# Performance work log

Measured on AMD Instinct MI355X. Metric: run time of the kernel, lower is better.

Reference implementation:

```python
import jax, jax.numpy as jnp
import numpy as np

N, E, G, L, D = 50000, 800000, 512, 3, 128
BN_EPS = 1e-5


def setup_inputs() -> dict:
    key = jax.random.key(0)
    ks = jax.random.split(key, 16)
    x = jax.random.normal(ks[0], (N, D), dtype=jnp.float32)
    edge_index = jax.random.randint(ks[1], (2, E), 0, N)
    batch = jnp.sort(jax.random.randint(ks[2], (N,), 0, G))
    W1 = jax.random.normal(ks[3], (L, D, D), dtype=jnp.float32) * 0.05
    b1 = jax.random.normal(ks[4], (L, D), dtype=jnp.float32) * 0.05
    gamma = jax.random.uniform(ks[5], (L, D), dtype=jnp.float32) + 0.5
    beta = jax.random.normal(ks[6], (L, D), dtype=jnp.float32) * 0.05
    running_mean = jax.random.normal(ks[7], (L, D), dtype=jnp.float32) * 0.1
    running_var = jax.random.uniform(ks[8], (L, D), dtype=jnp.float32) + 0.5
    W2 = jax.random.normal(ks[9], (L, D, D), dtype=jnp.float32) * 0.05
    b2 = jax.random.normal(ks[10], (L, D), dtype=jnp.float32) * 0.05
    lin1_W = jax.random.normal(ks[11], (L * D, L * D), dtype=jnp.float32) * 0.05
    lin1_b = jax.random.normal(ks[12], (L * D,), dtype=jnp.float32) * 0.05
    lin2_W = jax.random.normal(ks[13], (L * D, 10), dtype=jnp.float32) * 0.05
    lin2_b = jax.random.normal(ks[14], (10,), dtype=jnp.float32) * 0.05
    return {"x": x, "edge_index": edge_index, "batch": batch,
            "W1": W1, "b1": b1, "gamma": gamma, "beta": beta,
            "running_mean": running_mean, "running_var": running_var,
            "W2": W2, "b2": b2, "lin1_W": lin1_W, "lin1_b": lin1_b,
            "lin2_W": lin2_W, "lin2_b": lin2_b}


def _gin_layer(h, src, dst, W1, b1, gamma, beta, rm, rv, W2, b2):
    # GINConv (eps=0): MLP((1+eps)*x + sum_{j->i} x_j); aggregate src->dst
    agg = jax.ops.segment_sum(h[src], dst, num_segments=N)  # [N, D]
    z = (h + agg) @ W1 + b1
    # BatchNorm1d in eval mode (running stats)
    z = (z - rm) * (gamma / jnp.sqrt(rv + BN_EPS)) + beta
    z = jax.nn.relu(z)
    return jax.nn.relu(z @ W2 + b2)


def reference(x, edge_index, batch, W1, b1, gamma, beta, running_mean,
              running_var, W2, b2, lin1_W, lin1_b, lin2_W, lin2_b):
    src, dst = edge_index[0], edge_index[1]
    h = x
    pooled = []
    for i in range(L):
        h = _gin_layer(h, src, dst, W1[i], b1[i], gamma[i], beta[i],
                       running_mean[i], running_var[i], W2[i], b2[i])
        pooled.append(jax.ops.segment_sum(h, batch, num_segments=G))  # [G, D]
    g = jnp.concatenate(pooled, axis=1)  # [G, L*D]
    g = jax.nn.relu(g @ lin1_W + lin1_b)
    # dropout is identity in eval mode
    return g @ lin2_W + lin2_b  # [G, num_classes]
```

## Files before the change

kernel.cpp:

```cpp
#include <hip/hip_runtime.h>
#include <hip/hip_bf16.h>

#define D_FEAT 128
#define N_GRAPHS 512
#define N_LAYERS 3
#define POOL_DIM (N_LAYERS * D_FEAT)
#define N_CLASSES 10
#define BN_EPS 1e-5f
#define CAP 64
#define NBINS 8
#define SLABCAP 768
#define NSLICE 4


typedef __attribute__((ext_vector_type(8))) short bf16x8;
typedef __attribute__((ext_vector_type(8))) unsigned short ushort8;
typedef __attribute__((ext_vector_type(4))) float f32x4;

__device__ __forceinline__ unsigned short f2bf(float f) {
    unsigned u = __builtin_bit_cast(unsigned, f);
    u += 0x7FFFu + ((u >> 16) & 1u);
    return (unsigned short)(u >> 16);
}
__device__ __forceinline__ float bf2f(unsigned short h) {
    unsigned u = ((unsigned)h) << 16;
    return __builtin_bit_cast(float, u);
}
__device__ __forceinline__ float bf_lo(unsigned u) {
    return __builtin_bit_cast(float, u << 16);
}
__device__ __forceinline__ float bf_hi(unsigned u) {
    return __builtin_bit_cast(float, u & 0xffff0000u);
}

__global__ __launch_bounds__(256) void setup_kernel(
        const float* __restrict__ x, unsigned short* __restrict__ xb,
        const float* __restrict__ W1, const float* __restrict__ W2,
        unsigned short* __restrict__ Wt,
        const float* __restrict__ b1, const float* __restrict__ gamma,
        const float* __restrict__ beta, const float* __restrict__ rm,
        const float* __restrict__ rv, const float* __restrict__ b2,
        float* __restrict__ ea, float* __restrict__ eb,
        int* __restrict__ cursor, float* __restrict__ pooled,
        const int* __restrict__ ei, int2* __restrict__ pairs,
        int* __restrict__ cnts, int E,
        int N, int n4, int B0, int B1, int B2, int B3, int B4) {
    int b = blockIdx.x, tid = threadIdx.x;
    if (b < B0) {
        int i = b * 256 + tid;
        if (i < n4) {
            float4 v = ((const float4*)x)[i];
            ushort4 o;
            o.x = f2bf(v.x); o.y = f2bf(v.y); o.z = f2bf(v.z); o.w = f2bf(v.w);
            int node = i >> 5;
            int c4 = i & 31;
            int sl = c4 >> 3;
            int off = c4 & 7;
            ((ushort4*)xb)[((size_t)sl * N + node) * 8 + off] = o;
        }
    } else if (b < B1) {
        __shared__ float tile[64][65];
        int t = b - B0;
        int slot = t >> 2;
        int r0 = ((t >> 1) & 1) * 64;
        int c0 = (t & 1) * 64;
        int l = slot >> 1;
        const float* W = (slot & 1) ? W2 : W1;
        const float* Wb = W + (size_t)l * D_FEAT * D_FEAT;
        int rr = tid >> 2, cc4 = (tid & 3) * 16;
        #pragma unroll
        for (int j = 0; j < 16; ++j)
            tile[rr][cc4 + j] = Wb[(size_t)(r0 + rr) * D_FEAT + c0 + cc4 + j];
        __syncthreads();
        int nn = tid >> 2, kk4 = (tid & 3) * 16;
        unsigned short* Wo = Wt + (size_t)slot * D_FEAT * D_FEAT;
        #pragma unroll
        for (int j = 0; j < 16; ++j)
            Wo[(size_t)(c0 + nn) * D_FEAT + r0 + kk4 + j] = f2bf(tile[kk4 + j][nn]);
    } else if (b < B2) {
        int i = (b - B1) * 256 + tid;
        if (i < N_LAYERS * D_FEAT) {
            int l = i >> 7, c = i & 127;
            float s = gamma[i] * rsqrtf(rv[i] + BN_EPS);
            ea[(2 * l) * D_FEAT + c] = s;
            eb[(2 * l) * D_FEAT + c] = (b1[i] - rm[i]) * s + beta[i];
            ea[(2 * l + 1) * D_FEAT + c] = 1.0f;
            eb[(2 * l + 1) * D_FEAT + c] = b2[i];
        }
    } else if (b < B3) {
        int i = (b - B2) * 256 + tid;
        if (i < N) cursor[i] = 0;
    } else if (b < B4) {
        int i = (b - B3) * 256 + tid;
        if (i < N_GRAPHS * POOL_DIM) pooled[i] = 0.f;
    } else {
        __shared__ int loc[NBINS];
        int bb = b - B4;
        int per = (E + 255) / 256;
        int e0 = bb * per;
        int e1 = e0 + per; if (e1 > E) e1 = E;
        int span = (N + NBINS - 1) / NBINS;
        if (tid < NBINS) loc[tid] = 0;
        __syncthreads();
        for (int e = e0 + tid; e < e1; e += 256) {
            int dst = ei[E + e];
            int src = ei[e];
            int bin = dst / span;
            int p = atomicAdd(&loc[bin], 1);
            if (p < SLABCAP)
                pairs[((size_t)(bin * 256 + bb)) * SLABCAP + p] = make_int2(src, dst);
        }
        __syncthreads();
        if (tid < NBINS)
            cnts[tid * 256 + bb] = loc[tid];
    }
}

__global__ __launch_bounds__(256) void fill_v3(const int2* __restrict__ pairs,
                                               const int* __restrict__ cnts,
                                               int* __restrict__ cursor,
                                               unsigned short* __restrict__ bucket) {
    int r = blockIdx.x & 7;
    int chunk = blockIdx.x >> 3;
    #pragma unroll
    for (int s = 0; s < 4; ++s) {
        int blk = chunk * 4 + s;
        int cnt = cnts[r * 256 + blk];
        if (cnt > SLABCAP) cnt = SLABCAP;
        const int2* slab = pairs + (size_t)(r * 256 + blk) * SLABCAP;
        for (int p = threadIdx.x; p < cnt; p += 256) {
            int2 pr = slab[p];
            int pos = atomicAdd(&cursor[pr.y], 1);
            if (pos < CAP)
                bucket[(size_t)pr.y * CAP + pos] = (unsigned short)pr.x;
        }
    }
}

__global__ __launch_bounds__(256) void agg_slice(
        const unsigned short* __restrict__ hs,
        const int* __restrict__ deg,
        const unsigned short* __restrict__ bucket,
        unsigned short* __restrict__ ys,
        int n, int nchunks) {
    int xcd = blockIdx.x & 7;
    int s = xcd >> 1;
    int chunk = (blockIdx.x >> 3) * 2 + (xcd & 1);
    if (chunk >= nchunks) return;
    int wave = threadIdx.x >> 6, lane = threadIdx.x & 63;
    int grp = lane >> 2, sub = lane & 3;
    int n0 = chunk * 64 + wave * 16 + grp;
    bool valid = n0 < n;
    int node = valid ? n0 : 0;
    int d = valid ? deg[node] : 0;
    if (d > CAP) d = CAP;

    const uint4* h4 = (const uint4*)hs;
    size_t sbase = (size_t)s * n * 4;
    const unsigned short* brow = bucket + (size_t)node * CAP;

    int dmax = d;
    dmax = max(dmax, __shfl_xor(dmax, 4));
    dmax = max(dmax, __shfl_xor(dmax, 8));
    dmax = max(dmax, __shfl_xor(dmax, 16));
    dmax = max(dmax, __shfl_xor(dmax, 32));

    uint4 sv = h4[sbase + (size_t)node * 4 + sub];

    float acc[8] = {0.f,0.f,0.f,0.f,0.f,0.f,0.f,0.f};

    if (dmax > 0) {
        int sA[4];
        #pragma unroll
        for (int u = 0; u < 4; ++u) {
            sA[u] = node;
            if (u < d) sA[u] = (int)brow[u];
        }
        for (int t = 0; t < dmax; t += 4) {
            uint4 w[4];
            #pragma unroll
            for (int u = 0; u < 4; ++u) {
                w[u] = make_uint4(0u, 0u, 0u, 0u);
                if (t + u < d)
                    w[u] = h4[sbase + (size_t)sA[u] * 4 + sub];
            }
            int sB[4];
            #pragma unroll
            for (int u = 0; u < 4; ++u) {
                int e = t + 4 + u;
                sB[u] = node;
                if (e < d) sB[u] = (int)brow[e];
            }
            #pragma unroll
            for (int u = 0; u < 4; ++u) {
                uint4 v = w[u];
                acc[0] += bf_lo(v.x); acc[1] += bf_hi(v.x);
                acc[2] += bf_lo(v.y); acc[3] += bf_hi(v.y);
                acc[4] += bf_lo(v.z); acc[5] += bf_hi(v.z);
                acc[6] += bf_lo(v.w); acc[7] += bf_hi(v.w);
            }
            #pragma unroll
            for (int u = 0; u < 4; ++u) sA[u] = sB[u];
        }
    }

    acc[0] += bf_lo(sv.x); acc[1] += bf_hi(sv.x);
    acc[2] += bf_lo(sv.y); acc[3] += bf_hi(sv.y);
    acc[4] += bf_lo(sv.z); acc[5] += bf_hi(sv.z);
    acc[6] += bf_lo(sv.w); acc[7] += bf_hi(sv.w);

    if (valid) {
        uint4 o;
        o.x = (unsigned)f2bf(acc[0]) | ((unsigned)f2bf(acc[1]) << 16);
        o.y = (unsigned)f2bf(acc[2]) | ((unsigned)f2bf(acc[3]) << 16);
        o.z = (unsigned)f2bf(acc[4]) | ((unsigned)f2bf(acc[5]) << 16);
        o.w = (unsigned)f2bf(acc[6]) | ((unsigned)f2bf(acc[7]) << 16);
        ((uint4*)ys)[sbase + (size_t)node * 4 + sub] = o;
    }
}

__global__ __launch_bounds__(256) void layer_fused(const unsigned short* __restrict__ A,
                                                   const unsigned short* __restrict__ Wt1,
                                                   const unsigned short* __restrict__ Wt2,
                                                   const float* __restrict__ ea1,
                                                   const float* __restrict__ eb1,
                                                   const float* __restrict__ ea2,
                                                   const float* __restrict__ eb2,
                                                   const int* __restrict__ batch,
                                                   float* __restrict__ pooled, int loff,
                                                   unsigned short* __restrict__ outh, int n) {
    __shared__ unsigned short As[64][136];
    __shared__ unsigned short Ws[128][136];
    int tid = threadIdx.x;
    int row0 = blockIdx.x * 64;
    int wave = tid >> 6, lane = tid & 63;
    int m0 = wave * 16;
    int lrow = lane & 15, lq = lane >> 4;

    #pragma unroll
    for (int i = 0; i < 4; ++i) {
        int idx = tid + i * 256;
        int r = idx >> 4, c = (idx & 15) * 8;
        int sl = c >> 5, off = c & 31;
        ushort8 v = (ushort8)0;
        if (row0 + r < n)
            v = *(const ushort8*)&A[((size_t)sl * n + (row0 + r)) * 32 + off];
        *(ushort8*)&As[r][c] = v;
    }
    #pragma unroll
    for (int i = 0; i < 8; ++i) {
        int idx = tid + i * 256;
        int r = idx >> 4, c = (idx & 15) * 8;
        *(ushort8*)&Ws[r][c] = *(const ushort8*)&Wt1[(size_t)r * D_FEAT + c];
    }

    ushort8 w2reg[8];
    #pragma unroll
    for (int i = 0; i < 8; ++i) {
        int idx = tid + i * 256;
        int r = idx >> 4, c = (idx & 15) * 8;
        w2reg[i] = *(const ushort8*)&Wt2[(size_t)r * D_FEAT + c];
    }

    int gr0 = row0 + m0 + lq * 4;
    int bq[4];
    if (gr0 + 3 < n) {
        int4 b4 = *(const int4*)&batch[gr0];
        bq[0] = b4.x; bq[1] = b4.y; bq[2] = b4.z; bq[3] = b4.w;
    } else {
        #pragma unroll
        for (int r = 0; r < 4; ++r)
            bq[r] = (gr0 + r < n) ? batch[gr0 + r] : -1;
    }
    __syncthreads();

    f32x4 acc[8] = {};
    #pragma unroll
    for (int t = 0; t < 4; ++t) {
        bf16x8 a = *(const bf16x8*)&As[m0 + lrow][t * 32 + lq * 8];
        #pragma unroll
        for (int nt = 0; nt < 8; ++nt) {
            bf16x8 b = *(const bf16x8*)&Ws[nt * 16 + lrow][t * 32 + lq * 8];
            acc[nt] = __builtin_amdgcn_mfma_f32_16x16x32_bf16(a, b, acc[nt], 0, 0, 0);
        }
    }
    __syncthreads();

    #pragma unroll
    for (int nt = 0; nt < 8; ++nt) {
        int col = nt * 16 + lrow;
        float al = ea1[col], be = eb1[col];
        #pragma unroll
        for (int r = 0; r < 4; ++r) {
            float v = fmaxf(fmaf(acc[nt][r], al, be), 0.f);
            As[m0 + lq * 4 + r][col] = f2bf(v);
        }
    }
    #pragma unroll
    for (int i = 0; i < 8; ++i) {
        int idx = tid + i * 256;
        int r = idx >> 4, c = (idx & 15) * 8;
        *(ushort8*)&Ws[r][c] = w2reg[i];
    }
    __syncthreads();

    f32x4 acc2[8] = {};
    #pragma unroll
    for (int t = 0; t < 4; ++t) {
        bf16x8 a = *(const bf16x8*)&As[m0 + lrow][t * 32 + lq * 8];
        #pragma unroll
        for (int nt = 0; nt < 8; ++nt) {
            bf16x8 b = *(const bf16x8*)&Ws[nt * 16 + lrow][t * 32 + lq * 8];
            acc2[nt] = __builtin_amdgcn_mfma_f32_16x16x32_bf16(a, b, acc2[nt], 0, 0, 0);
        }
    }

    float vv[8][4];
    #pragma unroll
    for (int nt = 0; nt < 8; ++nt) {
        int col = nt * 16 + lrow;
        float al = ea2[col], be = eb2[col];
        int sl = col >> 5, off = col & 31;
        #pragma unroll
        for (int r = 0; r < 4; ++r) {
            unsigned short hb = f2bf(fmaxf(fmaf(acc2[nt][r], al, be), 0.f));
            vv[nt][r] = bf2f(hb);
            if (outh) {
                int grow = row0 + m0 + lq * 4 + r;
                if (grow < n)
                    outh[((size_t)sl * n + grow) * 32 + off] = hb;
            }
        }
    }

    int gmn = 0x7fffffff, gmx = -1;
    #pragma unroll
    for (int r = 0; r < 4; ++r) {
        if (bq[r] >= 0) {
            gmn = bq[r] < gmn ? bq[r] : gmn;
            gmx = bq[r] > gmx ? bq[r] : gmx;
        }
    }
    {
        int t;
        t = __shfl_xor(gmn, 16); gmn = t < gmn ? t : gmn;
        t = __shfl_xor(gmn, 32); gmn = t < gmn ? t : gmn;
        t = __shfl_xor(gmx, 16); gmx = t > gmx ? t : gmx;
        t = __shfl_xor(gmx, 32); gmx = t > gmx ? t : gmx;
    }
    for (int seg = gmn; seg <= gmx; ++seg) {
        #pragma unroll
        for (int nt = 0; nt < 8; ++nt) {
            float s = 0.f;
            #pragma unroll
            for (int r = 0; r < 4; ++r)
                if (bq[r] == seg) s += vv[nt][r];
            s += __shfl_xor(s, 16);
            s += __shfl_xor(s, 32);
            if (lq == 0 && s != 0.f)
                atomicAdd(&pooled[(size_t)seg * POOL_DIM + loff + nt * 16 + lrow], s);
        }
    }
}

__global__ __launch_bounds__(384) void head_kernel(const float* __restrict__ pooled,
                                                   const float* __restrict__ W1,
                                                   const float* __restrict__ b1v,
                                                   const float* __restrict__ W2,
                                                   const float* __restrict__ b2v,
                                                   float* __restrict__ out) {
    __shared__ float f1[4][POOL_DIM];
    int j = threadIdx.x;
    int g0 = blockIdx.x * 4;
    const float* pr = pooled + (size_t)g0 * POOL_DIM;
    float bb = b1v[j];
    float s0 = bb, s1 = bb, s2 = bb, s3 = bb;
    for (int k0 = 0; k0 < POOL_DIM; k0 += 8) {
        float w[8];
        #pragma unroll
        for (int i = 0; i < 8; ++i)
            w[i] = W1[(size_t)(k0 + i) * POOL_DIM + j];
        #pragma unroll
        for (int i = 0; i < 8; ++i) {
            int k = k0 + i;
            s0 = fmaf(pr[k],                w[i], s0);
            s1 = fmaf(pr[POOL_DIM + k],     w[i], s1);
            s2 = fmaf(pr[2 * POOL_DIM + k], w[i], s2);
            s3 = fmaf(pr[3 * POOL_DIM + k], w[i], s3);
        }
    }
    f1[0][j] = fmaxf(s0, 0.f);
    f1[1][j] = fmaxf(s1, 0.f);
    f1[2][j] = fmaxf(s2, 0.f);
    f1[3][j] = fmaxf(s3, 0.f);
    __syncthreads();
    if (j < 4 * N_CLASSES) {
        int g = j / N_CLASSES, c = j % N_CLASSES;
        float s = b2v[c];
        for (int k = 0; k < POOL_DIM; ++k)
            s = fmaf(f1[g][k], W2[(size_t)k * N_CLASSES + c], s);
        out[(size_t)(g0 + g) * N_CLASSES + c] = s;
    }
}

extern "C" void kernel_launch(void* const* d_in, const int* in_sizes, int n_in,
                              void* d_out, int out_size, void* d_ws, size_t ws_size,
                              hipStream_t stream) {
    const float* x      = (const float*)d_in[0];
    const int*   ei     = (const int*)  d_in[1];
    const int*   batch  = (const int*)  d_in[2];
    const float* W1     = (const float*)d_in[3];
    const float* b1     = (const float*)d_in[4];
    const float* gamma  = (const float*)d_in[5];
    const float* beta   = (const float*)d_in[6];
    const float* rm     = (const float*)d_in[7];
    const float* rv     = (const float*)d_in[8];
    const float* W2     = (const float*)d_in[9];
    const float* b2     = (const float*)d_in[10];
    const float* lin1W  = (const float*)d_in[11];
    const float* lin1b  = (const float*)d_in[12];
    const float* lin2W  = (const float*)d_in[13];
    const float* lin2b  = (const float*)d_in[14];
    float* out = (float*)d_out;

    const int N = in_sizes[0] / D_FEAT;
    const int E = in_sizes[1] / 2;

    char* ws = (char*)d_ws;
    auto carve = [&](size_t bytes) {
        char* p = ws;
        ws += (bytes + 255) & ~(size_t)255;
        return p;
    };
    int*   cursor    = (int*)  carve((size_t)N * 4);
    int*   cnts      = (int*)  carve((size_t)NBINS * 256 * 4);
    unsigned short* bucket = (unsigned short*)carve((size_t)N * CAP * 2);
    int2*  pairs     = (int2*) carve((size_t)NBINS * 256 * SLABCAP * 8);
    float* ea        = (float*)carve((size_t)2 * N_LAYERS * D_FEAT * 4);
    float* eb        = (float*)carve((size_t)2 * N_LAYERS * D_FEAT * 4);
    unsigned short* Wt   = (unsigned short*)carve((size_t)2 * N_LAYERS * D_FEAT * D_FEAT * 2);
    unsigned short* xb   = (unsigned short*)carve((size_t)N * D_FEAT * 2);
    unsigned short* ybuf = (unsigned short*)carve((size_t)N * D_FEAT * 2);
    unsigned short* hbuf = (unsigned short*)carve((size_t)N * D_FEAT * 2);
    float* pooled    = (float*)carve((size_t)N_GRAPHS * POOL_DIM * 4);

    const int n4 = N * D_FEAT / 4;
    const int B0 = (n4 + 255) / 256;
    const int B1 = B0 + 24;
    const int B2 = B1 + 2;
    const int B3 = B2 + (N + 255) / 256;
    const int B4 = B3 + (N_GRAPHS * POOL_DIM + 255) / 256;
    const int B5 = B4 + 256;

    setup_kernel<<<B5, 256, 0, stream>>>(x, xb, W1, W2, Wt, b1, gamma, beta,
                                         rm, rv, b2, ea, eb, cursor, pooled,
                                         ei, pairs, cnts, E,
                                         N, n4, B0, B1, B2, B3, B4);
    fill_v3<<<8 * 64, 256, 0, stream>>>(pairs, cnts, cursor, bucket);

    const int nchunks = (N + 63) / 64;
    const int gblocks = 8 * ((nchunks + 1) / 2);

    const unsigned short* hprev = xb;
    for (int l = 0; l < N_LAYERS; ++l) {
        agg_slice<<<gblocks, 256, 0, stream>>>(hprev, cursor, bucket, ybuf,
                                               N, nchunks);
        unsigned short* outh = (l == N_LAYERS - 1) ? nullptr : hbuf;
        layer_fused<<<(N + 63) / 64, 256, 0, stream>>>(ybuf,
                      Wt + (size_t)(2 * l) * D_FEAT * D_FEAT,
                      Wt + (size_t)(2 * l + 1) * D_FEAT * D_FEAT,
                      ea + (size_t)(2 * l) * D_FEAT,
                      eb + (size_t)(2 * l) * D_FEAT,
                      ea + (size_t)(2 * l + 1) * D_FEAT,
                      eb + (size_t)(2 * l + 1) * D_FEAT,
                      batch, pooled, l * D_FEAT, outh, N);
        hprev = hbuf;
    }
    head_kernel<<<N_GRAPHS / 4, 384, 0, stream>>>(pooled, lin1W, lin1b, lin2W, lin2b, out);
}
```

Measured before the change: 349.6 us.

## Use persistent grid in aggregation and load neighbor indices with one vector load plus shuffles

The aggregation kernel now runs a fixed grid of 2048 blocks that loop over chunks in a grid-stride fashion, keeping the XCD-to-slice mapping. Each lane loads 8 bucket indices with a single 16-byte load, and the first 32 neighbor ids are spread across the 4-lane group with shuffles, replacing scalar per-edge index loads. Degrees above 32 fall back to a serial scalar loop. The goal is to cut index-load latency and block launch overhead, at the cost of a serial tail and slightly more register pressure.

```diff
diff --git a/kernel.cpp b/kernel.cpp
--- a/kernel.cpp
+++ b/kernel.cpp
@@ -145,51 +145,44 @@
         int n, int nchunks) {
     int xcd = blockIdx.x & 7;
     int s = xcd >> 1;
-    int chunk = (blockIdx.x >> 3) * 2 + (xcd & 1);
-    if (chunk >= nchunks) return;
+    int worker = (blockIdx.x >> 3) * 2 + (xcd & 1);
     int wave = threadIdx.x >> 6, lane = threadIdx.x & 63;
     int grp = lane >> 2, sub = lane & 3;
-    int n0 = chunk * 64 + wave * 16 + grp;
-    bool valid = n0 < n;
-    int node = valid ? n0 : 0;
-    int d = valid ? deg[node] : 0;
-    if (d > CAP) d = CAP;
-
     const uint4* h4 = (const uint4*)hs;
     size_t sbase = (size_t)s * n * 4;
-    const unsigned short* brow = bucket + (size_t)node * CAP;
-
-    int dmax = d;
-    dmax = max(dmax, __shfl_xor(dmax, 4));
-    dmax = max(dmax, __shfl_xor(dmax, 8));
-    dmax = max(dmax, __shfl_xor(dmax, 16));
-    dmax = max(dmax, __shfl_xor(dmax, 32));
-
-    uint4 sv = h4[sbase + (size_t)node * 4 + sub];
-
-    float acc[8] = {0.f,0.f,0.f,0.f,0.f,0.f,0.f,0.f};
-
-    if (dmax > 0) {
-        int sA[4];
-        #pragma unroll
-        for (int u = 0; u < 4; ++u) {
-            sA[u] = node;
-            if (u < d) sA[u] = (int)brow[u];
-        }
-        for (int t = 0; t < dmax; t += 4) {
+
+    for (int chunk = worker; chunk < nchunks; chunk += 512) {
+        int n0 = chunk * 64 + wave * 16 + grp;
+        bool valid = n0 < n;
+        int node = valid ? n0 : 0;
+        int d = valid ? deg[node] : 0;
+        if (d > CAP) d = CAP;
+        const unsigned short* brow = bucket + (size_t)node * CAP;
+
+        uint4 iv = *(const uint4*)&brow[sub * 8];
+
+        uint4 sv = h4[sbase + (size_t)node * 4 + sub];
+
+        int dmax = d;
+        dmax = max(dmax, __shfl_xor(dmax, 4));
+        dmax = max(dmax, __shfl_xor(dmax, 8));
+        dmax = max(dmax, __shfl_xor(dmax, 16));
+        dmax = max(dmax, __shfl_xor(dmax, 32));
+
+        float acc[8] = {0.f,0.f,0.f,0.f,0.f,0.f,0.f,0.f};
+
+        auto do4 = [&](int e0, unsigned q0, unsigned q1) {
+            int id[4];
+            id[0] = (int)(q0 & 0xffffu);
+            id[1] = (int)(q0 >> 16);
+            id[2] = (int)(q1 & 0xffffu);
+            id[3] = (int)(q1 >> 16);
             uint4 w[4];
             #pragma unroll
             for (int u = 0; u < 4; ++u) {
                 w[u] = make_uint4(0u, 0u, 0u, 0u);
-                if (t + u < d)
-                    w[u] = h4[sbase + (size_t)sA[u] * 4 + sub];
-            }
-            int sB[4];
-            #pragma unroll
-            for (int u = 0; u < 4; ++u) {
-                int e = t + 4 + u;
-                sB[u] = node;
-                if (e < d) sB[u] = (int)brow[e];
+                if (e0 + u < d)
+                    w[u] = h4[sbase + (size_t)id[u] * 4 + sub];
             }
             #pragma unroll
             for (int u = 0; u < 4; ++u) {
@@ -199,23 +192,40 @@
                 acc[4] += bf_lo(v.z); acc[5] += bf_hi(v.z);
                 acc[6] += bf_lo(v.w); acc[7] += bf_hi(v.w);
             }
-            #pragma unroll
-            for (int u = 0; u < 4; ++u) sA[u] = sB[u];
-        }
-    }
-
-    acc[0] += bf_lo(sv.x); acc[1] += bf_hi(sv.x);
-    acc[2] += bf_lo(sv.y); acc[3] += bf_hi(sv.y);
-    acc[4] += bf_lo(sv.z); acc[5] += bf_hi(sv.z);
-    acc[6] += bf_lo(sv.w); acc[7] += bf_hi(sv.w);
-
-    if (valid) {
-        uint4 o;
-        o.x = (unsigned)f2bf(acc[0]) | ((unsigned)f2bf(acc[1]) << 16);
-        o.y = (unsigned)f2bf(acc[2]) | ((unsigned)f2bf(acc[3]) << 16);
-        o.z = (unsigned)f2bf(acc[4]) | ((unsigned)f2bf(acc[5]) << 16);
-        o.w = (unsigned)f2bf(acc[6]) | ((unsigned)f2bf(acc[7]) << 16);
-        ((uint4*)ys)[sbase + (size_t)node * 4 + sub] = o;
+        };
+
+        int dcap = dmax < 32 ? dmax : 32;
+        for (int t = 0; t < dcap; t += 8) {
+            int src = (grp << 2) + (t >> 3);
+            unsigned q0 = (unsigned)__shfl((int)iv.x, src);
+            unsigned q1 = (unsigned)__shfl((int)iv.y, src);
+            do4(t, q0, q1);
+            q0 = (unsigned)__shfl((int)iv.z, src);
+            q1 = (unsigned)__shfl((int)iv.w, src);
+            do4(t + 4, q0, q1);
+        }
+        for (int e = 32; e < d; ++e) {
+            int idx = (int)brow[e];
+            uint4 v = h4[sbase + (size_t)idx * 4 + sub];
+            acc[0] += bf_lo(v.x); acc[1] += bf_hi(v.x);
+            acc[2] += bf_lo(v.y); acc[3] += bf_hi(v.y);
+            acc[4] += bf_lo(v.z); acc[5] += bf_hi(v.z);
+            acc[6] += bf_lo(v.w); acc[7] += bf_hi(v.w);
+        }
+
+        acc[0] += bf_lo(sv.x); acc[1] += bf_hi(sv.x);
+        acc[2] += bf_lo(sv.y); acc[3] += bf_hi(sv.y);
+        acc[4] += bf_lo(sv.z); acc[5] += bf_hi(sv.z);
+        acc[6] += bf_lo(sv.w); acc[7] += bf_hi(sv.w);
+
+        if (valid) {
+            uint4 o;
+            o.x = (unsigned)f2bf(acc[0]) | ((unsigned)f2bf(acc[1]) << 16);
+            o.y = (unsigned)f2bf(acc[2]) | ((unsigned)f2bf(acc[3]) << 16);
+            o.z = (unsigned)f2bf(acc[4]) | ((unsigned)f2bf(acc[5]) << 16);
+            o.w = (unsigned)f2bf(acc[6]) | ((unsigned)f2bf(acc[7]) << 16);
+            ((uint4*)ys)[sbase + (size_t)node * 4 + sub] = o;
+        }
     }
 }
 
@@ -459,12 +469,11 @@
     fill_v3<<<8 * 64, 256, 0, stream>>>(pairs, cnts, cursor, bucket);
 
     const int nchunks = (N + 63) / 64;
-    const int gblocks = 8 * ((nchunks + 1) / 2);
 
     const unsigned short* hprev = xb;
     for (int l = 0; l < N_LAYERS; ++l) {
-        agg_slice<<<gblocks, 256, 0, stream>>>(hprev, cursor, bucket, ybuf,
-                                               N, nchunks);
+        agg_slice<<<2048, 256, 0, stream>>>(hprev, cursor, bucket, ybuf,
+                                            N, nchunks);
         unsigned short* outh = (l == N_LAYERS - 1) ? nullptr : hbuf;
         layer_fused<<<(N + 63) / 64, 256, 0, stream>>>(ybuf,
                       Wt + (size_t)(2 * l) * D_FEAT * D_FEAT,
```

New measurement: 304.4 us. 12.9% less time.
